# Kernel optimization log

Measured on AMD Instinct MI355X. Metric: run time of the kernel, lower is better.

The kernel has to match this reference:

```python
import jax, jax.numpy as jnp
import numpy as np

B, L, T = 32, 512, 48
START_ID, END_ID = 46, 47


def setup_inputs() -> dict:
    key = jax.random.key(0)
    kf, kt, ks = jax.random.split(key, 3)
    features = jax.random.normal(kf, (B, L, T), dtype=jnp.float32)
    transitions = jax.random.normal(kt, (T, T), dtype=jnp.float32) * 0.1
    seqLens = jax.random.randint(ks, (B,), 1, L + 1)  # lengths in [1, L]
    mask = jnp.arange(L)[None, :] < seqLens[:, None]  # [B, L] bool
    return {"features": features, "transitions": transitions,
            "seqLens": seqLens, "mask": mask}


def reference(features, transitions, seqLens, mask):
    # features: [B, L, T]; transitions: [T, T]
    Bv, Lv, Tv = features.shape
    # scores[b, t, i, j] = transitions[i, j] + features[b, t, i]
    scores = transitions[None, None, :, :] + features[:, :, :, None]  # [B,L,T,T]

    alpha0 = scores[:, 0, :, START_ID]  # [B, T] = trans[:, start] + feat[:, 0, :]

    def step(alpha_prev, s_t):
        # alpha_t[b, i] = logsumexp_j( alpha_{t-1}[b, j] + s_t[b, i, j] )
        a = jax.nn.logsumexp(alpha_prev[:, None, :] + s_t, axis=2)
        return a, a

    scores_t = jnp.swapaxes(scores, 0, 1)  # [L, B, T, T]
    _, alphas_rest = jax.lax.scan(step, alpha0, scores_t[1:])  # [L-1, B, T]
    alpha = jnp.concatenate([alpha0[None], alphas_rest], axis=0)  # [L, B, T]
    alpha = jnp.swapaxes(alpha, 0, 1)  # [B, L, T]

    # gather alpha at position seqLens-1 per batch element
    last = jnp.take_along_axis(alpha, (seqLens - 1)[:, None, None], axis=1)[:, 0, :]  # [B,T]
    last = last + transitions[END_ID][None, :]
    logZ = jnp.sum(jax.nn.logsumexp(last, axis=1))  # scalar
    return logZ, scores
```

## Files before the change

kernel.cpp:

```cpp
#include <hip/hip_runtime.h>

#define BB 32
#define LL 512
#define TT 48
#define START_ID 46
#define END_ID 47

constexpr int   BLT  = BB * LL * TT;
constexpr unsigned NSC = 37748736u;
constexpr unsigned NGRP = 9437183u;

constexpr int SEGS   = 31;
constexpr int SEGLEN = 16;
constexpr int GW     = 1152;
constexpr int NSEG   = BB * SEGS;
constexpr int SOFF   = NSEG * GW;
constexpr int ZOFF   = SOFF + NSEG;
constexpr int ZFOFF  = ZOFF + 32;
constexpr size_t WS_NEED = (size_t)(ZFOFF + 32) * 4;

typedef __fp16 f16x2 __attribute__((ext_vector_type(2)));
typedef __fp16 f16x8 __attribute__((ext_vector_type(8)));
typedef float  f32x4 __attribute__((ext_vector_type(4)));
typedef unsigned u32x4 __attribute__((ext_vector_type(4)));

__device__ __forceinline__ float fexp2(float x) { return __builtin_amdgcn_exp2f(x); }
__device__ __forceinline__ float flog2(float x) { return __builtin_amdgcn_logf(x); }
__device__ __forceinline__ float rfirst(float x) {
  return __uint_as_float(__builtin_amdgcn_readfirstlane(__float_as_uint(x)));
}
__device__ __forceinline__ float fdot2(f16x2 a, f16x2 b, float c) {
  return __builtin_amdgcn_fdot2(a, b, c, false);
}
__device__ __forceinline__ f16x2 bc(unsigned u) { return __builtin_bit_cast(f16x2, u); }
__device__ __forceinline__ unsigned pk2(float a, float b) {
  return __builtin_bit_cast(unsigned, __builtin_amdgcn_cvt_pkrtz(a, b));
}
__device__ __forceinline__ float dpp_xor1(float x) {
  return __int_as_float(__builtin_amdgcn_update_dpp(
      __float_as_int(x), __float_as_int(x), 0xB1, 0xF, 0xF, true));
}
__device__ __forceinline__ f16x8 b8(unsigned d0, unsigned d1) {
  u32x4 u; u.x = d0; u.y = d1; u.z = 0u; u.w = 0u;
  return __builtin_bit_cast(f16x8, u);
}
__device__ __forceinline__ f32x4 MF(f16x8 a, f16x8 b, f32x4 c) {
  return __builtin_amdgcn_mfma_f32_16x16x32_f16(a, b, c, 0, 0, 0);
}
__device__ __forceinline__ unsigned magicv(unsigned i) {
  return 0x5EC0DE5Au + i * 2654435761u;
}

#define GLD16(gp, lp)                                                        \
  __builtin_amdgcn_global_load_lds(                                          \
      (const __attribute__((address_space(1))) unsigned int*)(gp),           \
      (__attribute__((address_space(3))) unsigned int*)(lp), 16, 0, 0)

__device__ __attribute__((noinline)) void crf_tree_body(
    const float* __restrict__ feat, const float* __restrict__ trans,
    float* __restrict__ ws, float* lds, int wg, int lane)
{
  constexpr float LOG2E = 1.4426950408889634f;
  unsigned* gws = (unsigned*)ws;
  const int b  = wg / SEGS, s = wg - b * SEGS;
  const int col = lane & 15, grp = lane >> 4, rb = grp * 4;

  const char* gbase = (const char*)feat + (size_t)b * 98304 + (size_t)(SEGLEN * s + 1) * 192;
#pragma unroll
  for (int w = 0; w < 3; ++w)
    GLD16(gbase + w * 1024 + lane * 16, (char*)lds + w * 1024);

  float4 T_[3][3];
#pragma unroll
  for (int I = 0; I < 3; ++I)
#pragma unroll
    for (int K = 0; K < 3; ++K) {
      const float4 t4 = *(const float4*)(trans + (I * 16 + col) * 48 + K * 16 + rb);
      T_[I][K].x = fexp2(t4.x * LOG2E);
      T_[I][K].y = fexp2(t4.y * LOG2E);
      T_[I][K].z = fexp2(t4.z * LOG2E);
      T_[I][K].w = fexp2(t4.w * LOG2E);
    }

  unsigned Bd[3][3][2];
#pragma unroll
  for (int K = 0; K < 3; ++K)
#pragma unroll
    for (int J = 0; J < 3; ++J) {
      const float b0 = (K == J && rb + 0 == col) ? 1.f : 0.f;
      const float b1 = (K == J && rb + 1 == col) ? 1.f : 0.f;
      const float b2 = (K == J && rb + 2 == col) ? 1.f : 0.f;
      const float b3 = (K == J && rb + 3 == col) ? 1.f : 0.f;
      Bd[K][J][0] = pk2(b0, b1);
      Bd[K][J][1] = pk2(b2, b3);
    }

  asm volatile("s_waitcnt vmcnt(0)" ::: "memory");
  __builtin_amdgcn_sched_barrier(0);

  float km = 0.f, Sacc = 0.f;
  f32x4 C[3][3];
  const f32x4 zz = {0.f, 0.f, 0.f, 0.f};

  for (int p = 0; p < SEGLEN; ++p) {
    Sacc += km;
    float ef[3];
    ef[0] = fexp2(fmaf(lds[p * 48 +  0 + col], LOG2E, -km));
    ef[1] = fexp2(fmaf(lds[p * 48 + 16 + col], LOG2E, -km));
    ef[2] = fexp2(fmaf(lds[p * 48 + 32 + col], LOG2E, -km));
    f16x8 A_[3][3];
#pragma unroll
    for (int I = 0; I < 3; ++I)
#pragma unroll
      for (int K = 0; K < 3; ++K) {
        u32x4 u;
        u.x = pk2(T_[I][K].x * ef[I], T_[I][K].y * ef[I]);
        u.y = pk2(T_[I][K].z * ef[I], T_[I][K].w * ef[I]);
        u.z = 0u; u.w = 0u;
        A_[I][K] = __builtin_bit_cast(f16x8, u);
      }
#pragma unroll
    for (int I = 0; I < 3; ++I)
#pragma unroll
      for (int J = 0; J < 3; ++J) {
        f32x4 c = MF(A_[I][0], b8(Bd[0][J][0], Bd[0][J][1]), zz);
        c = MF(A_[I][1], b8(Bd[1][J][0], Bd[1][J][1]), c);
        c = MF(A_[I][2], b8(Bd[2][J][0], Bd[2][J][1]), c);
        C[I][J] = c;
      }
    const unsigned u00 = __builtin_amdgcn_readfirstlane(__float_as_uint(C[0][0][0]));
    km = (float)((int)((u00 >> 23) & 255u) - 127);
#pragma unroll
    for (int K = 0; K < 3; ++K)
#pragma unroll
      for (int J = 0; J < 3; ++J) {
        Bd[K][J][0] = pk2(C[K][J][0], C[K][J][1]);
        Bd[K][J][1] = pk2(C[K][J][2], C[K][J][3]);
      }
  }

  const unsigned gb = (unsigned)wg * GW;
#pragma unroll
  for (int I = 0; I < 3; ++I)
#pragma unroll
    for (int J = 0; J < 3; ++J)
#pragma unroll
      for (int r = 0; r < 4; ++r) {
        const float cn = dpp_xor1(C[I][J][r]);
        const unsigned pk = pk2(C[I][J][r], cn);
        if (!(col & 1))
          gws[gb + (unsigned)((I * 16 + rb + r) * 24 + ((J * 16 + col) >> 1))] = pk;
      }
  if (lane == 0) ws[SOFF + wg] = Sacc;
}

__global__ __launch_bounds__(64) void crf_tree_kernel(
    const float* __restrict__ feat, const float* __restrict__ trans,
    float* __restrict__ ws)
{
  __shared__ __align__(16) float fls[SEGLEN * 48];
  crf_tree_body(feat, trans, ws, fls, blockIdx.x, threadIdx.x);
}

__device__ __attribute__((noinline)) void crf_phaseB(
    const float* __restrict__ feat, const float* __restrict__ trans,
    const int* __restrict__ seqLens, float* __restrict__ ws, int b, int lane)
{
  constexpr float LOG2E = 1.4426950408889634f;
  constexpr float LN2   = 0.6931471805599453f;
  const unsigned* gws = (const unsigned*)ws;
  const int ii = lane < 47 ? lane : 47;
  const int Lb = seqLens[b];
  const int steps = Lb - 1;
  const int nfull = steps >> 4;

  f16x2 E00,E01,E02,E03,E04,E05,E06,E07,E08,E09,E10,E11,
        E12,E13,E14,E15,E16,E17,E18,E19,E20,E21,E22,E23;
#define LDE(V, J) { const float e0_ = fexp2(trans[ii*48 + 2*(J)]     * LOG2E); \
                    const float e1_ = fexp2(trans[ii*48 + 2*(J) + 1] * LOG2E); \
                    V = __builtin_amdgcn_cvt_pkrtz(e0_, e1_); }
  LDE(E00,0)  LDE(E01,1)  LDE(E02,2)  LDE(E03,3)  LDE(E04,4)  LDE(E05,5)
  LDE(E06,6)  LDE(E07,7)  LDE(E08,8)  LDE(E09,9)  LDE(E10,10) LDE(E11,11)
  LDE(E12,12) LDE(E13,13) LDE(E14,14) LDE(E15,15) LDE(E16,16) LDE(E17,17)
  LDE(E18,18) LDE(E19,19) LDE(E20,20) LDE(E21,21) LDE(E22,22) LDE(E23,23)
#undef LDE
  const float tS = trans[ii * 48 + START_ID];
  const float tE = trans[END_ID * 48 + ii];
  const float* fb = feat + (size_t)b * (LL * TT);

  const float a0 = (tS + fb[ii]) * LOG2E;
  const float anch = rfirst(a0);
  float v = fexp2(a0 - anch);
  float sigma = anch;

#define RL24                                                               \
        unsigned s00,s01,s02,s03,s04,s05,s06,s07,s08,s09,s10,s11,          \
                 s12,s13,s14,s15,s16,s17,s18,s19,s20,s21,s22,s23;          \
        s00=__builtin_amdgcn_readlane(pku,0);  s01=__builtin_amdgcn_readlane(pku,2);  \
        s02=__builtin_amdgcn_readlane(pku,4);  s03=__builtin_amdgcn_readlane(pku,6);  \
        s04=__builtin_amdgcn_readlane(pku,8);  s05=__builtin_amdgcn_readlane(pku,10); \
        s06=__builtin_amdgcn_readlane(pku,12); s07=__builtin_amdgcn_readlane(pku,14); \
        s08=__builtin_amdgcn_readlane(pku,16); s09=__builtin_amdgcn_readlane(pku,18); \
        s10=__builtin_amdgcn_readlane(pku,20); s11=__builtin_amdgcn_readlane(pku,22); \
        s12=__builtin_amdgcn_readlane(pku,24); s13=__builtin_amdgcn_readlane(pku,26); \
        s14=__builtin_amdgcn_readlane(pku,28); s15=__builtin_amdgcn_readlane(pku,30); \
        s16=__builtin_amdgcn_readlane(pku,32); s17=__builtin_amdgcn_readlane(pku,34); \
        s18=__builtin_amdgcn_readlane(pku,36); s19=__builtin_amdgcn_readlane(pku,38); \
        s20=__builtin_amdgcn_readlane(pku,40); s21=__builtin_amdgcn_readlane(pku,42); \
        s22=__builtin_amdgcn_readlane(pku,44); s23=__builtin_amdgcn_readlane(pku,46);

  const unsigned* grow = gws + (size_t)(b * SEGS) * GW + ii * 24;
  u32x4 h0,h1,h2,h3,h4,h5, n0,n1,n2,n3,n4,n5;
  if (nfull > 0) {
    const u32x4* gp = (const u32x4*)grow;
    h0 = gp[0]; h1 = gp[1]; h2 = gp[2]; h3 = gp[3]; h4 = gp[4]; h5 = gp[5];
  }
  for (int s = 0; s < nfull; ++s) {
    if (s + 1 < nfull) {
      const u32x4* gp = (const u32x4*)(grow + (size_t)(s + 1) * GW);
      n0 = gp[0]; n1 = gp[1]; n2 = gp[2]; n3 = gp[3]; n4 = gp[4]; n5 = gp[5];
    }
    const float pn = dpp_xor1(v);
    const unsigned pku = pk2(v, pn);
    RL24
    float d0, d1, d2, d3;
    d0 = fdot2(bc(h0.x), bc(s00), 0.0f);
    d1 = fdot2(bc(h0.y), bc(s01), 0.0f);
    d2 = fdot2(bc(h0.z), bc(s02), 0.0f);
    d3 = fdot2(bc(h0.w), bc(s03), 0.0f);
    d0 = fdot2(bc(h1.x), bc(s04), d0);
    d1 = fdot2(bc(h1.y), bc(s05), d1);
    d2 = fdot2(bc(h1.z), bc(s06), d2);
    d3 = fdot2(bc(h1.w), bc(s07), d3);
    d0 = fdot2(bc(h2.x), bc(s08), d0);
    d1 = fdot2(bc(h2.y), bc(s09), d1);
    d2 = fdot2(bc(h2.z), bc(s10), d2);
    d3 = fdot2(bc(h2.w), bc(s11), d3);
    d0 = fdot2(bc(h3.x), bc(s12), d0);
    d1 = fdot2(bc(h3.y), bc(s13), d1);
    d2 = fdot2(bc(h3.z), bc(s14), d2);
    d3 = fdot2(bc(h3.w), bc(s15), d3);
    d0 = fdot2(bc(h4.x), bc(s16), d0);
    d1 = fdot2(bc(h4.y), bc(s17), d1);
    d2 = fdot2(bc(h4.z), bc(s18), d2);
    d3 = fdot2(bc(h4.w), bc(s19), d3);
    d0 = fdot2(bc(h5.x), bc(s20), d0);
    d1 = fdot2(bc(h5.y), bc(s21), d1);
    d2 = fdot2(bc(h5.z), bc(s22), d2);
    d3 = fdot2(bc(h5.w), bc(s23), d3);
    const float dot = (d0 + d1) + (d2 + d3);
    const unsigned ub = __builtin_amdgcn_readfirstlane(__float_as_uint(dot));
    const int e = (int)((ub >> 23) & 255u) - 127;
    v = dot * __uint_as_float((unsigned)(127 - e) << 23);
    sigma += (float)e + ws[SOFF + b * SEGS + s];
    h0 = n0; h1 = n1; h2 = n2; h3 = n3; h4 = n4; h5 = n5;
  }

  int t = nfull * 16 + 1;
  if (t <= steps) {
    float f_cur = fb[(size_t)t * 48 + ii];
    for (; t <= steps; ++t) {
      const int tn = (t + 1 <= steps) ? t + 1 : t;
      const float f_nxt = fb[(size_t)tn * 48 + ii];
      const float pn = dpp_xor1(v);
      const unsigned pku = pk2(v, pn);
      RL24
      float d0, d1, d2, d3;
      d0 = fdot2(E00, bc(s00), 0.0f);
      d1 = fdot2(E01, bc(s01), 0.0f);
      d2 = fdot2(E02, bc(s02), 0.0f);
      d3 = fdot2(E03, bc(s03), 0.0f);
      d0 = fdot2(E04, bc(s04), d0);
      d1 = fdot2(E05, bc(s05), d1);
      d2 = fdot2(E06, bc(s06), d2);
      d3 = fdot2(E07, bc(s07), d3);
      d0 = fdot2(E08, bc(s08), d0);
      d1 = fdot2(E09, bc(s09), d1);
      d2 = fdot2(E10, bc(s10), d2);
      d3 = fdot2(E11, bc(s11), d3);
      d0 = fdot2(E12, bc(s12), d0);
      d1 = fdot2(E13, bc(s13), d1);
      d2 = fdot2(E14, bc(s14), d2);
      d3 = fdot2(E15, bc(s15), d3);
      d0 = fdot2(E16, bc(s16), d0);
      d1 = fdot2(E17, bc(s17), d1);
      d2 = fdot2(E18, bc(s18), d2);
      d3 = fdot2(E19, bc(s19), d3);
      d0 = fdot2(E20, bc(s20), d0);
      d1 = fdot2(E21, bc(s21), d1);
      d2 = fdot2(E22, bc(s22), d2);
      d3 = fdot2(E23, bc(s23), d3);
      const float dot = (d0 + d1) + (d2 + d3);
      const float w = dot * fexp2(f_cur * LOG2E);
      const unsigned ub = __builtin_amdgcn_readfirstlane(__float_as_uint(w));
      const int e = (int)((ub >> 23) & 255u) - 127;
      v = w * __uint_as_float((unsigned)(127 - e) << 23);
      sigma += (float)e;
      f_cur = f_nxt;
    }
  }
#undef RL24

  float contrib = (lane < 48) ? v * fexp2(tE * LOG2E) : 0.0f;
#pragma unroll
  for (int off = 32; off; off >>= 1) contrib += __shfl_xor(contrib, off, 64);
  if (lane == 0) ws[ZOFF + b] = (flog2(contrib) + sigma) * LN2;
  __threadfence();
  if (lane == 0)
    __hip_atomic_store((unsigned*)ws + ZFOFF + b, magicv((unsigned)(NSEG + b)),
                       __ATOMIC_RELAXED, __HIP_MEMORY_SCOPE_AGENT);
}

__device__ __forceinline__ void scores_writer_rng(
    const float* __restrict__ feat, float* __restrict__ out,
    float* lds, unsigned k, unsigned kstride, unsigned kend)
{
  for (; k < kend; k += kstride) {
    const unsigned idx = 3u + 4u * k;
    const unsigned r0 = idx / 48u;
    const unsigned j0 = idx - r0 * 48u;
    const unsigned i0 = r0 % 48u;
    const unsigned rn = (r0 + 1u < (unsigned)BLT) ? r0 + 1u : (unsigned)(BLT - 1);
    const float fa = feat[r0];
    const float fn = feat[rn];
    const unsigned i1 = (i0 + 1u < 48u) ? i0 + 1u : 0u;
    float v[4];
#pragma unroll
    for (int e = 0; e < 4; ++e) {
      const unsigned j = j0 + (unsigned)e;
      const bool wr = j >= 48u;
      const unsigned jj = wr ? j - 48u : j;
      v[e] = (wr ? fn : fa) + lds[(wr ? i1 : i0) * 48u + jj];
    }
    float4 o; o.x = v[0]; o.y = v[1]; o.z = v[2]; o.w = v[3];
    *(float4*)(out + 4u + 4u * (size_t)k) = o;
  }
}

__global__ __launch_bounds__(256) void crf_fusedB_kernel(
    const float* __restrict__ feat, const float* __restrict__ trans,
    const int* __restrict__ seqLens, float* __restrict__ out,
    float* __restrict__ ws)
{
  __shared__ __align__(16) float lds[2304];
  const int blk = blockIdx.x;
  const int tid = threadIdx.x;

  if (blk < BB) {
    const int b = blk;
    if (tid >= 64) {
      if (b == 0) {
        if (tid <= 66) out[tid - 63] = feat[0] + trans[tid - 64];
        else if (tid == 67) out[NSC] = feat[BLT - 1] + trans[2303];
      }
      return;
    }
    crf_phaseB(feat, trans, seqLens, ws, b, tid);
    if (b == 0) {
      const unsigned* zf = (const unsigned*)ws + ZFOFF;
      if (tid > 0 && tid < 32) {
        const unsigned want = magicv((unsigned)(NSEG + tid));
        while (__hip_atomic_load(zf + tid, __ATOMIC_RELAXED, __HIP_MEMORY_SCOPE_AGENT) != want)
          __builtin_amdgcn_s_sleep(2);
      }
      __threadfence();
      float v = (tid < 32) ? ws[ZOFF + tid] : 0.0f;
#pragma unroll
      for (int off = 32; off; off >>= 1) v += __shfl_xor(v, off, 64);
      if (tid == 0) out[0] = v;
    }
    return;
  }

  for (int s = tid; s < 2304; s += 256) lds[s] = trans[s];
  __syncthreads();
  scores_writer_rng(feat, out, lds,
                    (unsigned)(blk - BB) * 256u + tid,
                    (gridDim.x - BB) * 256u, NGRP);
}

__device__ __attribute__((noinline)) void crf_recursion_body(
    const float* __restrict__ feat, const float* __restrict__ trans,
    const int* __restrict__ seqLens, float* __restrict__ ws,
    float* lds, int blk, int lane)
{
  constexpr float LOG2E = 1.4426950408889634f;
  const int ii = lane < 47 ? lane : 47;
  const char* gbase = (const char*)(feat + (size_t)blk * (LL * TT));
  const int Lb = seqLens[blk];

#pragma unroll
  for (int w = 0; w < 6; ++w)
    GLD16(gbase + w * 1024 + lane * 16, (char*)&lds[0] + w * 1024);

  f16x2 E00,E01,E02,E03,E04,E05,E06,E07,E08,E09,E10,E11,
        E12,E13,E14,E15,E16,E17,E18,E19,E20,E21,E22,E23;
#define LDE(V, J) { const float e0_ = fexp2(trans[ii*48 + 2*(J)]     * LOG2E); \
                    const float e1_ = fexp2(trans[ii*48 + 2*(J) + 1] * LOG2E); \
                    V = __builtin_amdgcn_cvt_pkrtz(e0_, e1_); }
  LDE(E00,0)  LDE(E01,1)  LDE(E02,2)  LDE(E03,3)  LDE(E04,4)  LDE(E05,5)
  LDE(E06,6)  LDE(E07,7)  LDE(E08,8)  LDE(E09,9)  LDE(E10,10) LDE(E11,11)
  LDE(E12,12) LDE(E13,13) LDE(E14,14) LDE(E15,15) LDE(E16,16) LDE(E17,17)
  LDE(E18,18) LDE(E19,19) LDE(E20,20) LDE(E21,21) LDE(E22,22) LDE(E23,23)
#undef LDE
  const float tS = trans[ii * 48 + START_ID];
  const float tE = trans[END_ID * 48 + ii];

  asm volatile("s_waitcnt vmcnt(0)" ::: "memory");
  __builtin_amdgcn_sched_barrier(0);

  const float f00 = lds[ii];
  float a2 = (tS + f00) * LOG2E;
  float M2 = rfirst(a2) + 5.0f;

  const int nch = (Lb + 31) >> 5;
  for (int c = 0; c < nch; ++c) {
    const bool pre = (c + 1 < nch);
    if (pre) {
      const char* g = gbase + (size_t)(c + 1) * 6144;
      char* l = (char*)&lds[((c + 1) & 1) * 1536];
#pragma unroll
      for (int w = 0; w < 6; ++w) GLD16(g + w * 1024 + lane * 16, l + w * 1024);
    }
    const int tend = ((c + 1) * 32 < Lb) ? (c + 1) * 32 : Lb;
    const int t0 = (c == 0 ? 1 : c * 32);
    const int base = (c & 1) * 1536 + ii;
    if (t0 < tend) {
      float f_cur = lds[base + (t0 - c * 32) * 48];
      for (int t = t0; t < tend; ++t) {
        const int lnxt = ((t + 1 < tend) ? t + 1 : t) - c * 32;
        const float f_nxt = lds[base + lnxt * 48];
        const float p  = fexp2(a2 - M2);
        const float pn = dpp_xor1(p);
        const unsigned pku = pk2(p, pn);
        unsigned s00,s01,s02,s03,s04,s05,s06,s07,s08,s09,s10,s11,
                 s12,s13,s14,s15,s16,s17,s18,s19,s20,s21,s22,s23;
#define RL(K) __builtin_amdgcn_readlane(pku, (K))
        s00=RL(0);  s01=RL(2);  s02=RL(4);  s03=RL(6);
        s04=RL(8);  s05=RL(10); s06=RL(12); s07=RL(14);
        s08=RL(16); s09=RL(18); s10=RL(20); s11=RL(22);
        s12=RL(24); s13=RL(26); s14=RL(28); s15=RL(30);
        s16=RL(32); s17=RL(34); s18=RL(36); s19=RL(38);
        s20=RL(40); s21=RL(42); s22=RL(44); s23=RL(46);
#undef RL
        float d0, d1, d2, d3;
        d0 = fdot2(E00, bc(s00), 0.0f);
        d1 = fdot2(E01, bc(s01), 0.0f);
        d2 = fdot2(E02, bc(s02), 0.0f);
        d3 = fdot2(E03, bc(s03), 0.0f);
        d0 = fdot2(E04, bc(s04), d0);
        d1 = fdot2(E05, bc(s05), d1);
        d2 = fdot2(E06, bc(s06), d2);
        d3 = fdot2(E07, bc(s07), d3);
        d0 = fdot2(E08, bc(s08), d0);
        d1 = fdot2(E09, bc(s09), d1);
        d2 = fdot2(E10, bc(s10), d2);
        d3 = fdot2(E11, bc(s11), d3);
        d0 = fdot2(E12, bc(s12), d0);
        d1 = fdot2(E13, bc(s13), d1);
        d2 = fdot2(E14, bc(s14), d2);
        d3 = fdot2(E15, bc(s15), d3);
        d0 = fdot2(E16, bc(s16), d0);
        d1 = fdot2(E17, bc(s17), d1);
        d2 = fdot2(E18, bc(s18), d2);
        d3 = fdot2(E19, bc(s19), d3);
        d0 = fdot2(E20, bc(s20), d0);
        d1 = fdot2(E21, bc(s21), d1);
        d2 = fdot2(E22, bc(s22), d2);
        d3 = fdot2(E23, bc(s23), d3);
        const float dot = (d0 + d1) + (d2 + d3);
        a2 = fmaf(f_cur, LOG2E, M2 + flog2(dot));
        M2 = rfirst(a2) + 5.0f;
        f_cur = f_nxt;
      }
    }
    asm volatile("s_waitcnt vmcnt(0)" ::: "memory");
    __builtin_amdgcn_sched_barrier(0);
  }

  float last2 = (lane < 48) ? (a2 + tE * LOG2E) : -3.0e38f;
  float m2 = last2;
#pragma unroll
  for (int off = 32; off; off >>= 1) m2 = fmaxf(m2, __shfl_xor(m2, off, 64));
  float e = (lane < 48) ? fexp2(last2 - m2) : 0.0f;
#pragma unroll
  for (int off = 32; off; off >>= 1) e += __shfl_xor(e, off, 64);
  if (lane == 0) ws[blk] = (m2 + flog2(e)) * 0.6931471805599453f;
}

__global__ __launch_bounds__(256) void crf_fused2_kernel(
    const float* __restrict__ feat, const float* __restrict__ trans,
    const int* __restrict__ seqLens, float* __restrict__ out,
    float* __restrict__ ws)
{
  __shared__ __align__(16) float lds[3072];
  const int blk = blockIdx.x;
  if (blk < BB) {
    if (threadIdx.x >= 64) return;
    crf_recursion_body(feat, trans, seqLens, ws, lds, blk, threadIdx.x);
    return;
  }
  for (int s = threadIdx.x; s < 2304; s += 256) lds[s] = trans[s];
  __syncthreads();
  scores_writer_rng(feat, out, lds,
                    (unsigned)(blk - BB) * 256u + threadIdx.x,
                    (gridDim.x - BB) * 256u, NGRP);
}

__global__ void crf_finalize_kernel(const float* __restrict__ feat,
                                    const float* __restrict__ trans,
                                    const float* __restrict__ zws,
                                    float* __restrict__ out)
{
  const int t = threadIdx.x;
  float v = (t < 32) ? zws[t] : 0.0f;
#pragma unroll
  for (int off = 32; off; off >>= 1) v += __shfl_xor(v, off, 64);
  if (t == 0) out[0] = v;
  else if (t <= 3) out[t] = feat[0] + trans[t - 1];
  else if (t == 4) out[NSC] = feat[BLT - 1] + trans[2303];
}

extern "C" void kernel_launch(void* const* d_in, const int* in_sizes, int n_in,
                              void* d_out, int out_size, void* d_ws, size_t ws_size,
                              hipStream_t stream) {
  const float* feat    = (const float*)d_in[0];
  const float* trans   = (const float*)d_in[1];
  const int*   seqLens = (const int*)d_in[2];
  float* out = (float*)d_out;
  float* ws  = (float*)d_ws;

  if (ws_size >= WS_NEED) {
    hipLaunchKernelGGL(crf_tree_kernel, dim3(NSEG), dim3(64), 0, stream,
                       feat, trans, ws);
    hipLaunchKernelGGL(crf_fusedB_kernel, dim3(2048), dim3(256), 0, stream,
                       feat, trans, seqLens, out, ws);
  } else {
    hipLaunchKernelGGL(crf_fused2_kernel, dim3(2048), dim3(256), 0, stream,
                       feat, trans, seqLens, out, ws);
    hipLaunchKernelGGL(crf_finalize_kernel, dim3(1), dim3(64), 0, stream,
                       feat, trans, ws, out);
  }
}
```

Baseline: 66.04 us.

## Use 16x16x16 MFMA, nontemporal score stores, and separate finalize kernel

```diff
diff --git a/kernel.cpp b/kernel.cpp
--- a/kernel.cpp
+++ b/kernel.cpp
@@ -16,12 +16,12 @@
 constexpr int NSEG   = BB * SEGS;
 constexpr int SOFF   = NSEG * GW;
 constexpr int ZOFF   = SOFF + NSEG;
-constexpr int ZFOFF  = ZOFF + 32;
-constexpr size_t WS_NEED = (size_t)(ZFOFF + 32) * 4;
+constexpr size_t WS_NEED = (size_t)(ZOFF + 32) * 4;
 
 typedef __fp16 f16x2 __attribute__((ext_vector_type(2)));
-typedef __fp16 f16x8 __attribute__((ext_vector_type(8)));
+typedef __fp16 f16x4 __attribute__((ext_vector_type(4)));
 typedef float  f32x4 __attribute__((ext_vector_type(4)));
+typedef unsigned u32x2 __attribute__((ext_vector_type(2)));
 typedef unsigned u32x4 __attribute__((ext_vector_type(4)));
 
 __device__ __forceinline__ float fexp2(float x) { return __builtin_amdgcn_exp2f(x); }
@@ -40,15 +40,12 @@
   return __int_as_float(__builtin_amdgcn_update_dpp(
       __float_as_int(x), __float_as_int(x), 0xB1, 0xF, 0xF, true));
 }
-__device__ __forceinline__ f16x8 b8(unsigned d0, unsigned d1) {
-  u32x4 u; u.x = d0; u.y = d1; u.z = 0u; u.w = 0u;
-  return __builtin_bit_cast(f16x8, u);
-}
-__device__ __forceinline__ f32x4 MF(f16x8 a, f16x8 b, f32x4 c) {
-  return __builtin_amdgcn_mfma_f32_16x16x32_f16(a, b, c, 0, 0, 0);
-}
-__device__ __forceinline__ unsigned magicv(unsigned i) {
-  return 0x5EC0DE5Au + i * 2654435761u;
+__device__ __forceinline__ f16x4 b4(unsigned d0, unsigned d1) {
+  u32x2 u; u.x = d0; u.y = d1;
+  return __builtin_bit_cast(f16x4, u);
+}
+__device__ __forceinline__ f32x4 MF16(f16x4 a, f16x4 b, f32x4 c) {
+  return __builtin_amdgcn_mfma_f32_16x16x16f16(a, b, c, 0, 0, 0);
 }
 
 #define GLD16(gp, lp)                                                        \
@@ -108,24 +105,21 @@
     ef[0] = fexp2(fmaf(lds[p * 48 +  0 + col], LOG2E, -km));
     ef[1] = fexp2(fmaf(lds[p * 48 + 16 + col], LOG2E, -km));
     ef[2] = fexp2(fmaf(lds[p * 48 + 32 + col], LOG2E, -km));
-    f16x8 A_[3][3];
+    unsigned Ad[3][3][2];
 #pragma unroll
     for (int I = 0; I < 3; ++I)
 #pragma unroll
       for (int K = 0; K < 3; ++K) {
-        u32x4 u;
-        u.x = pk2(T_[I][K].x * ef[I], T_[I][K].y * ef[I]);
-        u.y = pk2(T_[I][K].z * ef[I], T_[I][K].w * ef[I]);
-        u.z = 0u; u.w = 0u;
-        A_[I][K] = __builtin_bit_cast(f16x8, u);
+        Ad[I][K][0] = pk2(T_[I][K].x * ef[I], T_[I][K].y * ef[I]);
+        Ad[I][K][1] = pk2(T_[I][K].z * ef[I], T_[I][K].w * ef[I]);
       }
 #pragma unroll
     for (int I = 0; I < 3; ++I)
 #pragma unroll
       for (int J = 0; J < 3; ++J) {
-        f32x4 c = MF(A_[I][0], b8(Bd[0][J][0], Bd[0][J][1]), zz);
-        c = MF(A_[I][1], b8(Bd[1][J][0], Bd[1][J][1]), c);
-        c = MF(A_[I][2], b8(Bd[2][J][0], Bd[2][J][1]), c);
+        f32x4 c = MF16(b4(Ad[I][0][0], Ad[I][0][1]), b4(Bd[0][J][0], Bd[0][J][1]), zz);
+        c = MF16(b4(Ad[I][1][0], Ad[I][1][1]), b4(Bd[1][J][0], Bd[1][J][1]), c);
+        c = MF16(b4(Ad[I][2][0], Ad[I][2][1]), b4(Bd[2][J][0], Bd[2][J][1]), c);
         C[I][J] = c;
       }
     const unsigned u00 = __builtin_amdgcn_readfirstlane(__float_as_uint(C[0][0][0]));
@@ -305,10 +299,6 @@
 #pragma unroll
   for (int off = 32; off; off >>= 1) contrib += __shfl_xor(contrib, off, 64);
   if (lane == 0) ws[ZOFF + b] = (flog2(contrib) + sigma) * LN2;
-  __threadfence();
-  if (lane == 0)
-    __hip_atomic_store((unsigned*)ws + ZFOFF + b, magicv((unsigned)(NSEG + b)),
-                       __ATOMIC_RELAXED, __HIP_MEMORY_SCOPE_AGENT);
 }
 
 __device__ __forceinline__ void scores_writer_rng(
@@ -332,8 +322,8 @@
       const unsigned jj = wr ? j - 48u : j;
       v[e] = (wr ? fn : fa) + lds[(wr ? i1 : i0) * 48u + jj];
     }
-    float4 o; o.x = v[0]; o.y = v[1]; o.z = v[2]; o.w = v[3];
-    *(float4*)(out + 4u + 4u * (size_t)k) = o;
+    f32x4 o; o.x = v[0]; o.y = v[1]; o.z = v[2]; o.w = v[3];
+    __builtin_nontemporal_store(o, (f32x4*)(out + 4u + 4u * (size_t)k));
   }
 }
 
@@ -344,39 +334,30 @@
 {
   __shared__ __align__(16) float lds[2304];
   const int blk = blockIdx.x;
-  const int tid = threadIdx.x;
-
   if (blk < BB) {
-    const int b = blk;
-    if (tid >= 64) {
-      if (b == 0) {
-        if (tid <= 66) out[tid - 63] = feat[0] + trans[tid - 64];
-        else if (tid == 67) out[NSC] = feat[BLT - 1] + trans[2303];
-      }
-      return;
-    }
-    crf_phaseB(feat, trans, seqLens, ws, b, tid);
-    if (b == 0) {
-      const unsigned* zf = (const unsigned*)ws + ZFOFF;
-      if (tid > 0 && tid < 32) {
-        const unsigned want = magicv((unsigned)(NSEG + tid));
-        while (__hip_atomic_load(zf + tid, __ATOMIC_RELAXED, __HIP_MEMORY_SCOPE_AGENT) != want)
-          __builtin_amdgcn_s_sleep(2);
-      }
-      __threadfence();
-      float v = (tid < 32) ? ws[ZOFF + tid] : 0.0f;
-#pragma unroll
-      for (int off = 32; off; off >>= 1) v += __shfl_xor(v, off, 64);
-      if (tid == 0) out[0] = v;
-    }
+    if (threadIdx.x >= 64) return;
+    crf_phaseB(feat, trans, seqLens, ws, blk, threadIdx.x);
     return;
   }
-
-  for (int s = tid; s < 2304; s += 256) lds[s] = trans[s];
+  for (int s = threadIdx.x; s < 2304; s += 256) lds[s] = trans[s];
   __syncthreads();
   scores_writer_rng(feat, out, lds,
-                    (unsigned)(blk - BB) * 256u + tid,
+                    (unsigned)(blk - BB) * 256u + threadIdx.x,
                     (gridDim.x - BB) * 256u, NGRP);
+}
+
+__global__ void crf_finalize_kernel(const float* __restrict__ feat,
+                                    const float* __restrict__ trans,
+                                    const float* __restrict__ zws,
+                                    float* __restrict__ out)
+{
+  const int t = threadIdx.x;
+  float v = (t < 32) ? zws[t] : 0.0f;
+#pragma unroll
+  for (int off = 32; off; off >>= 1) v += __shfl_xor(v, off, 64);
+  if (t == 0) out[0] = v;
+  else if (t <= 3) out[t] = feat[0] + trans[t - 1];
+  else if (t == 4) out[NSC] = feat[BLT - 1] + trans[2303];
 }
 
 __device__ __attribute__((noinline)) void crf_recursion_body(
@@ -507,20 +488,6 @@
                     (gridDim.x - BB) * 256u, NGRP);
 }
 
-__global__ void crf_finalize_kernel(const float* __restrict__ feat,
-                                    const float* __restrict__ trans,
-                                    const float* __restrict__ zws,
-                                    float* __restrict__ out)
-{
-  const int t = threadIdx.x;
-  float v = (t < 32) ? zws[t] : 0.0f;
-#pragma unroll
-  for (int off = 32; off; off >>= 1) v += __shfl_xor(v, off, 64);
-  if (t == 0) out[0] = v;
-  else if (t <= 3) out[t] = feat[0] + trans[t - 1];
-  else if (t == 4) out[NSC] = feat[BLT - 1] + trans[2303];
-}
-
 extern "C" void kernel_launch(void* const* d_in, const int* in_sizes, int n_in,
                               void* d_out, int out_size, void* d_ws, size_t ws_size,
                               hipStream_t stream) {
@@ -535,6 +502,8 @@
                        feat, trans, ws);
     hipLaunchKernelGGL(crf_fusedB_kernel, dim3(2048), dim3(256), 0, stream,
                        feat, trans, seqLens, out, ws);
+    hipLaunchKernelGGL(crf_finalize_kernel, dim3(1), dim3(64), 0, stream,
+                       feat, trans, ws + ZOFF, out);
   } else {
     hipLaunchKernelGGL(crf_fused2_kernel, dim3(2048), dim3(256), 0, stream,
                        feat, trans, seqLens, out, ws);
```

Result: faster. 57.49 us (-12.9%).
